# Kernel optimization log

Measured on AMD Instinct MI355X. Metric: run time of the kernel, lower is better.

The kernel has to match this reference:

```python
import math
import jax, jax.numpy as jnp
import numpy as np

DIM = 1024
NUM_HEADS = 16
HEAD_DIM = DIM // NUM_HEADS


def rotate_half(x):
    x1, x2 = jnp.split(x, 2, axis=-1)
    return jnp.concatenate((-x2, x1), axis=-1)


def rope_cos_sin(seq_len, head_dim, dtype):
    # angles: (S, D/2); duplicated to (S, D) so it applies to full head_dim
    pos = jnp.arange(seq_len, dtype=dtype)[:, None]
    inv = jnp.exp(jnp.arange(0, head_dim, 2, dtype=dtype) * (-(math.log(10000.0) / head_dim)))
    angles = pos * inv[None, :]
    angles = jnp.concatenate((angles, angles), axis=-1)  # (S, D)
    return jnp.cos(angles), jnp.sin(angles)


def setup_inputs() -> dict:
    key = jax.random.key(0)
    ks = jax.random.split(key, 5)
    B, S, C = 8, 1024, DIM
    scale = 1.0 / math.sqrt(C)
    return {
        "x": jax.random.normal(ks[0], (B, S, C), dtype=jnp.float32),
        "W_qkv": jax.random.normal(ks[1], (C, 3 * C), dtype=jnp.float32) * scale,
        "b_qkv": jax.random.normal(ks[2], (3 * C,), dtype=jnp.float32) * 0.02,
        "W_proj": jax.random.normal(ks[3], (C, C), dtype=jnp.float32) * scale,
        "b_proj": jax.random.normal(ks[4], (C,), dtype=jnp.float32) * 0.02,
    }


def reference(x, W_qkv, b_qkv, W_proj, b_proj):
    B, S, C = x.shape
    H, D = NUM_HEADS, C // NUM_HEADS
    scale = D ** -0.5

    qkv = x @ W_qkv + b_qkv                       # (B, S, 3C)
    qkv = qkv.reshape(B, S, 3, H, D).transpose(2, 0, 3, 1, 4)  # (3, B, H, S, D)
    q, k, v = qkv[0], qkv[1], qkv[2]

    cos, sin = rope_cos_sin(S, D, x.dtype)        # (S, D) each, broadcast over B,H
    q = q * cos + rotate_half(q) * sin
    k = k * cos + rotate_half(k) * sin

    attn = jnp.einsum("bhqd,bhkd->bhqk", q, k) * scale
    attn = jax.nn.softmax(attn, axis=-1)
    out = jnp.einsum("bhqk,bhkd->bhqd", attn, v)  # (B, H, S, D)
    out = out.transpose(0, 2, 1, 3).reshape(B, S, C)
    return out @ W_proj + b_proj
```

## Files before the change

### kernel.cpp

```cpp
#include <hip/hip_runtime.h>
#include <hip/hip_fp16.h>
#include <math.h>


typedef _Float16 half_t;
typedef _Float16 half8 __attribute__((ext_vector_type(8)));
typedef _Float16 half4v __attribute__((ext_vector_type(4)));
typedef float f32x4 __attribute__((ext_vector_type(4)));

#define MFMA16(a, b, c) __builtin_amdgcn_mfma_f32_16x16x32_f16(a, b, c, 0, 0, 0)

__device__ __forceinline__ void gload_lds16(const half_t* g, half_t* lds) {
  __builtin_amdgcn_global_load_lds(
      (const __attribute__((address_space(1))) void*)g,
      (__attribute__((address_space(3))) void*)lds, 16, 0, 0);
}

__device__ __forceinline__ void prep_transpose(const float* __restrict__ in,
                                               half_t* __restrict__ out,
                                               int rows, int cols, int bx,
                                               int by, half_t (*tile)[33]) {
  int c0 = bx * 32, r0 = by * 32;
  int tx = threadIdx.x & 31, g = threadIdx.x >> 5;
#pragma unroll
  for (int i = 0; i < 4; i++) {
    int r = g * 4 + i;
    tile[r][tx] = (half_t)in[(size_t)(r0 + r) * cols + c0 + tx];
  }
  __syncthreads();
#pragma unroll
  for (int i = 0; i < 4; i++) {
    int cc = g * 4 + i;
    out[(size_t)(c0 + cc) * rows + r0 + tx] = tile[tx][cc];
  }
}

__global__ __launch_bounds__(256) void k_prep(
    const float* __restrict__ x, half_t* __restrict__ x16,
    const float* __restrict__ Wqkv, half_t* __restrict__ WqkvT,
    const float* __restrict__ Wproj, half_t* __restrict__ WprojT,
    float2* __restrict__ rope) {
  __shared__ half_t tile[32][33];
  int bid = blockIdx.x;
  if (bid < 8192) {
    int i = bid * 256 + threadIdx.x;
    float4 v = ((const float4*)x)[i];
    half4v h;
    h.x = (half_t)v.x; h.y = (half_t)v.y; h.z = (half_t)v.z; h.w = (half_t)v.w;
    ((half4v*)x16)[i] = h;
  } else if (bid < 11264) {
    int idx = bid - 8192;
    prep_transpose(Wqkv, WqkvT, 1024, 3072, idx % 96, idx / 96, tile);
  } else if (bid < 12288) {
    int idx = bid - 11264;
    prep_transpose(Wproj, WprojT, 1024, 1024, idx & 31, idx >> 5, tile);
  } else {
    int idx = (bid - 12288) * 256 + threadIdx.x;
    int s = idx >> 5, jj = idx & 31;
    float inv = expf(-0.28782313662425572f * (float)jj);
    float ang = (float)s * inv;
    float sn, cs;
    sincosf(ang, &sn, &cs);
    rope[idx] = make_float2(cs, sn);
  }
}

template <int MODE>
__global__ __launch_bounds__(256) void k_gemm(
    const half_t* __restrict__ A, const half_t* __restrict__ Bt,
    const float* __restrict__ bias, const float2* __restrict__ rope,
    half_t* __restrict__ Qo, half_t* __restrict__ Ko, half_t* __restrict__ Vo,
    float* __restrict__ Fo) {
  __shared__ alignas(16) half_t smem[17408];
  half_t* As = smem;
  half_t* Bs = smem + 8192;
  const int t = threadIdx.x;
  const int lane = t & 63, w = t >> 6;
  const int quad = lane >> 4, cl = lane & 15;
  const int m0 = blockIdx.y * 128, n0 = blockIdx.x * 128;
  const int wm = (w >> 1) * 64, wn = (w & 1) * 64;

  f32x4 acc[4][4] = {};

  for (int kt = 0; kt < 1024; kt += 64) {
    __syncthreads();
#pragma unroll
    for (int cc = 0; cc < 4; cc++) {
      int lg = (w * 4 + cc) * 64 + lane;
      int row = lg >> 3;
      int gs = (lg & 7) ^ (row & 7);
      gload_lds16(A + (size_t)(m0 + row) * 1024 + kt + gs * 8,
                  As + (w * 4 + cc) * 512);
      gload_lds16(Bt + (size_t)(n0 + row) * 1024 + kt + gs * 8,
                  Bs + (w * 4 + cc) * 512);
    }
    __syncthreads();
#pragma unroll
    for (int ks = 0; ks < 2; ks++) {
      half8 af[4], bf[4];
#pragma unroll
      for (int i = 0; i < 4; i++) {
        int mr = wm + i * 16 + cl;
        af[i] = *(const half8*)(As + mr * 64 + (((ks * 4 + quad) ^ (mr & 7)) * 8));
        int nr = wn + i * 16 + cl;
        bf[i] = *(const half8*)(Bs + nr * 64 + (((ks * 4 + quad) ^ (nr & 7)) * 8));
      }
#pragma unroll
      for (int i = 0; i < 4; i++)
#pragma unroll
        for (int j = 0; j < 4; j++) acc[i][j] = MFMA16(af[i], bf[j], acc[i][j]);
    }
  }

  if (MODE == 0) {
    const int which = n0 >> 10;
    if (which == 2) {
      __syncthreads();
      half_t* T = smem;
#pragma unroll
      for (int i = 0; i < 4; i++)
#pragma unroll
        for (int j = 0; j < 4; j++)
#pragma unroll
          for (int r = 0; r < 4; r++) {
            int n = n0 + wn + j * 16 + cl;
            T[(wn + j * 16 + cl) * 136 + (wm + i * 16 + quad * 4 + r)] =
                (half_t)(acc[i][j][r] + bias[n]);
          }
      __syncthreads();
      const int b = m0 >> 10, sbase = m0 & 1023;
#pragma unroll
      for (int u = 0; u < 8; u++) {
        int ci = u * 256 + t;
        int drow = ci >> 4, scol = (ci & 15) * 8;
        half8 val = *(const half8*)(T + drow * 136 + scol);
        int n = n0 + drow;
        int hh = (n >> 6) & 15, d = n & 63;
        *(half8*)(Vo + ((size_t)((b * 16 + hh) * 64 + d)) * 1024 + sbase + scol) = val;
      }
    } else {
      __syncthreads();
      half_t* T = smem;
      const float qsc = (which == 0) ? 0.125f : 1.0f;
#pragma unroll
      for (int i = 0; i < 4; i++)
#pragma unroll
        for (int r = 0; r < 4; r++) {
          int ml = wm + i * 16 + quad * 4 + r;
          int s = (m0 + ml) & 1023;
#pragma unroll
          for (int j = 0; j < 4; j++) {
            int nl = wn + j * 16 + cl;
            int n = n0 + nl;
            int d = n & 63;
            float v = acc[i][j][r] + bias[n];
            float pr = acc[i][j ^ 2][r] + bias[n ^ 32];
            float2 tr = rope[(s << 5) | (d & 31)];
            float rv = (d < 32) ? (v * tr.x - pr * tr.y) : (v * tr.x + pr * tr.y);
            T[ml * 136 + nl] = (half_t)(rv * qsc);
          }
        }
      __syncthreads();
      half_t* dst = (which == 0) ? Qo : Ko;
      const int b = m0 >> 10;
#pragma unroll
      for (int u = 0; u < 8; u++) {
        int ci = u * 256 + t;
        int mrow = ci >> 4, ch = ci & 15;
        half8 val = *(const half8*)(T + mrow * 136 + ch * 8);
        int s = (m0 + mrow) & 1023;
        int n = n0 + ch * 8;
        int hh = (n >> 6) & 15, d = n & 63;
        *(half8*)(dst + ((size_t)((b * 16 + hh) * 1024 + s)) * 64 + d) = val;
      }
    }
  } else {
#pragma unroll
    for (int i = 0; i < 4; i++)
#pragma unroll
      for (int r = 0; r < 4; r++) {
        int gm = m0 + wm + i * 16 + quad * 4 + r;
#pragma unroll
        for (int j = 0; j < 4; j++) {
          int n = n0 + wn + j * 16 + cl;
          Fo[(size_t)gm * 1024 + n] = acc[i][j][r] + bias[n];
        }
      }
  }
}

__global__ __launch_bounds__(256) void k_attn(const half_t* __restrict__ Qg_,
                                              const half_t* __restrict__ Kg_,
                                              const half_t* __restrict__ Vg_,
                                              half_t* __restrict__ Og) {
  __shared__ alignas(16) half_t Qs[8192];
  __shared__ alignas(16) half_t Ks[4096];
  __shared__ alignas(16) half_t Vs[4096];
  __shared__ alignas(16) half_t Ps[128 * 72];
  __shared__ float ilbuf[128];
  const int t = threadIdx.x, lane = t & 63, w = t >> 6;
  const int quad = lane >> 4, cl = lane & 15;
  const int bh = blockIdx.x, q0 = blockIdx.y * 128;
  const half_t* Qg = Qg_ + (size_t)bh * 65536;
  const half_t* Kg = Kg_ + (size_t)bh * 65536;
  const half_t* Vg = Vg_ + (size_t)bh * 65536;

#pragma unroll
  for (int cc = 0; cc < 4; cc++) {
    int lg = (w * 4 + cc) * 64 + lane;
    int row = lg >> 3;
    int gs = (lg & 7) ^ (row & 7);
    gload_lds16(Qg + (size_t)(q0 + row) * 64 + gs * 8, Qs + (w * 4 + cc) * 512);
  }
  __syncthreads();

  half8 qf[2][2];
#pragma unroll
  for (int ks = 0; ks < 2; ks++)
#pragma unroll
    for (int j = 0; j < 2; j++) {
      int qr = w * 32 + j * 16 + cl;
      qf[ks][j] = *(const half8*)(Qs + qr * 64 + (((ks * 4 + quad) ^ (qr & 7)) * 8));
    }

  f32x4 oacc[2][4] = {};
  float lsum[2] = {0.f, 0.f};

  for (int kt = 0; kt < 1024; kt += 64) {
    __syncthreads();
#pragma unroll
    for (int cc = 0; cc < 2; cc++) {
      int lg = (w * 2 + cc) * 64 + lane;
      int row = lg >> 3;
      int gs = (lg & 7) ^ (row & 7);
      gload_lds16(Kg + (size_t)(kt + row) * 64 + gs * 8, Ks + (w * 2 + cc) * 512);
      gload_lds16(Vg + (size_t)row * 1024 + kt + gs * 8, Vs + (w * 2 + cc) * 512);
    }
    __syncthreads();

    f32x4 sacc[4][2] = {};
#pragma unroll
    for (int ks = 0; ks < 2; ks++) {
      half8 kf[4];
#pragma unroll
      for (int i = 0; i < 4; i++) {
        int kr = i * 16 + cl;
        kf[i] = *(const half8*)(Ks + kr * 64 + (((ks * 4 + quad) ^ (kr & 7)) * 8));
      }
#pragma unroll
      for (int i = 0; i < 4; i++)
#pragma unroll
        for (int j = 0; j < 2; j++)
          sacc[i][j] = MFMA16(kf[i], qf[ks][j], sacc[i][j]);
    }

#pragma unroll
    for (int i = 0; i < 4; i++)
#pragma unroll
      for (int j = 0; j < 2; j++) {
        float p0 = __expf(sacc[i][j][0] - 8.f);
        float p1 = __expf(sacc[i][j][1] - 8.f);
        float p2 = __expf(sacc[i][j][2] - 8.f);
        float p3 = __expf(sacc[i][j][3] - 8.f);
        lsum[j] += (p0 + p1) + (p2 + p3);
        half4v pk;
        pk.x = (half_t)p0; pk.y = (half_t)p1; pk.z = (half_t)p2; pk.w = (half_t)p3;
        *(half4v*)(Ps + (w * 32 + j * 16 + cl) * 72 + i * 16 + quad * 4) = pk;
      }

#pragma unroll
    for (int ks = 0; ks < 2; ks++) {
      half8 pf[2], vf[4];
#pragma unroll
      for (int i = 0; i < 2; i++)
        pf[i] = *(const half8*)(Ps + (w * 32 + i * 16 + cl) * 72 + ks * 32 + quad * 8);
#pragma unroll
      for (int j = 0; j < 4; j++) {
        int dr = j * 16 + cl;
        vf[j] = *(const half8*)(Vs + dr * 64 + (((ks * 4 + quad) ^ (dr & 7)) * 8));
      }
#pragma unroll
      for (int i = 0; i < 2; i++)
#pragma unroll
        for (int j = 0; j < 4; j++) oacc[i][j] = MFMA16(pf[i], vf[j], oacc[i][j]);
    }
  }

#pragma unroll
  for (int j = 0; j < 2; j++) {
    float l = lsum[j];
    l += __shfl_xor(l, 16);
    l += __shfl_xor(l, 32);
    if (quad == 0) ilbuf[w * 32 + j * 16 + cl] = 1.f / l;
  }

  const int b = bh >> 4, hh = bh & 15;
#pragma unroll
  for (int i = 0; i < 2; i++)
#pragma unroll
    for (int r = 0; r < 4; r++) {
      float sc = ilbuf[w * 32 + i * 16 + quad * 4 + r];
      int srow = q0 + w * 32 + i * 16 + quad * 4 + r;
#pragma unroll
      for (int j = 0; j < 4; j++) {
        int d = j * 16 + cl;
        Og[((size_t)(b * 1024 + srow)) * 1024 + hh * 64 + d] =
            (half_t)(oacc[i][j][r] * sc);
      }
    }
}

extern "C" void kernel_launch(void* const* d_in, const int* in_sizes, int n_in,
                              void* d_out, int out_size, void* d_ws,
                              size_t ws_size, hipStream_t stream) {
  (void)in_sizes; (void)n_in; (void)out_size; (void)ws_size;
  const float* x = (const float*)d_in[0];
  const float* Wqkv = (const float*)d_in[1];
  const float* bqkv = (const float*)d_in[2];
  const float* Wproj = (const float*)d_in[3];
  const float* bproj = (const float*)d_in[4];
  float* out = (float*)d_out;

  half_t* ws = (half_t*)d_ws;
  half_t* x16 = ws;
  half_t* WqkvT = ws + 8388608;
  half_t* WprojT = ws + 11534336;
  half_t* Q16 = ws + 12582912;
  half_t* K16 = ws + 20971520;
  half_t* V16 = ws + 29360128;
  float2* rope = (float2*)(ws + 37748736);
  half_t* O16 = x16;

  k_prep<<<12416, 256, 0, stream>>>(x, x16, Wqkv, WqkvT, Wproj, WprojT, rope);
  k_gemm<0><<<dim3(24, 64), 256, 0, stream>>>(x16, WqkvT, bqkv, rope, Q16, K16,
                                              V16, nullptr);
  k_attn<<<dim3(128, 8), 256, 0, stream>>>(Q16, K16, V16, O16);
  k_gemm<1><<<dim3(8, 64), 256, 0, stream>>>(O16, WprojT, bproj, nullptr,
                                             nullptr, nullptr, nullptr, out);
}
```

Baseline: 246.9 us.

## Replace QKV GEMM with 256x256-tile double-buffered 512-thread kernel

Adds a dedicated QKV projection kernel that uses 256x256 output tiles with 8 waves per block. It double-buffers K-slices in LDS via direct global-to-LDS loads interleaved with the MFMA phases, and remaps blocks to a swizzled grid order for L2 locality. The goal is more data reuse per loaded byte and overlap of loads with MFMA compute than the old 128x128 single-buffered GEMM. In exchange it uses 128 KB of LDS and many more accumulator registers, and the epilogue is split into two halves through LDS.

```diff
diff --git a/kernel.cpp b/kernel.cpp
--- a/kernel.cpp
+++ b/kernel.cpp
@@ -65,6 +65,159 @@
   }
 }
 
+
+#define STAGE_HALF(TT, PH)                                                   \
+  {                                                                          \
+    const int op_ = (PH) & 1, kh_ = (PH) >> 1;                               \
+    const half_t* src_ = op_ ? Bt : A;                                       \
+    const int r0_ = op_ ? n0 : m0;                                           \
+    half_t* reg_ = smem + (((TT) & 1) * 32768) + op_ * 16384 + kh_ * 8192;   \
+    _Pragma("unroll") for (int c_ = 0; c_ < 2; ++c_) {                       \
+      int gid_ = c_ * 512 + w * 64 + lane;                                   \
+      int row_ = gid_ >> 2, gi_ = gid_ & 3;                                  \
+      int sg_ = gi_ ^ ((row_ >> 1) & 3);                                     \
+      gload_lds16(src_ + (size_t)(r0_ + row_) * 1024 + (TT) * 64 +           \
+                      kh_ * 32 + sg_ * 8,                                    \
+                  reg_ + (c_ * 512 + w * 64) * 8);                           \
+    }                                                                        \
+  }
+
+__global__ __launch_bounds__(512, 2) void k_qkv(
+    const half_t* __restrict__ A, const half_t* __restrict__ Bt,
+    const float* __restrict__ bias, const float2* __restrict__ rope,
+    half_t* __restrict__ Qo, half_t* __restrict__ Ko,
+    half_t* __restrict__ Vo) {
+  __shared__ alignas(16) half_t smem[65536];
+  const int t = threadIdx.x;
+  const int lane = t & 63, w = t >> 6;
+  const int quad = lane >> 4, cl = lane & 15;
+  const int wr = w >> 2, wc = w & 3;
+
+  const int bid = blockIdx.x;
+  const int wg = (bid & 7) * 48 + (bid >> 3);
+  const int m0 = (wg & 31) * 256, n0 = (wg >> 5) * 256;
+
+#pragma unroll
+  for (int ph = 0; ph < 4; ++ph) STAGE_HALF(0, ph);
+  asm volatile("s_waitcnt vmcnt(4)" ::: "memory");
+  __builtin_amdgcn_s_barrier();
+
+  f32x4 acc[8][4] = {};
+  half8 bf[4];
+
+  for (int tt = 0; tt < 16; ++tt) {
+    half_t* Ab = smem + (tt & 1) * 32768;
+    half_t* Bb = Ab + 16384;
+#pragma unroll
+    for (int ph = 0; ph < 4; ++ph) {
+      const int ks = ph >> 1, mh = ph & 1;
+      if (mh == 0) {
+#pragma unroll
+        for (int j = 0; j < 4; ++j) {
+          int nr = wc * 64 + j * 16 + cl;
+          bf[j] = *(const half8*)(Bb + ks * 8192 + nr * 32 +
+                                  ((quad ^ ((nr >> 1) & 3)) * 8));
+        }
+      }
+      half8 af[4];
+#pragma unroll
+      for (int i = 0; i < 4; ++i) {
+        int mr = wr * 128 + mh * 64 + i * 16 + cl;
+        af[i] = *(const half8*)(Ab + ks * 8192 + mr * 32 +
+                                ((quad ^ ((mr >> 1) & 3)) * 8));
+      }
+      if (tt < 15) STAGE_HALF(tt + 1, ph);
+      __builtin_amdgcn_s_barrier();
+      asm volatile("s_waitcnt lgkmcnt(0)" ::: "memory");
+      __builtin_amdgcn_sched_barrier(0);
+      __builtin_amdgcn_s_setprio(1);
+#pragma unroll
+      for (int i = 0; i < 4; ++i)
+#pragma unroll
+        for (int j = 0; j < 4; ++j)
+          acc[mh * 4 + i][j] = MFMA16(af[i], bf[j], acc[mh * 4 + i][j]);
+      __builtin_amdgcn_s_setprio(0);
+      if (ph & 1) {
+        if (tt < 15)
+          asm volatile("s_waitcnt vmcnt(4)" ::: "memory");
+        else
+          asm volatile("s_waitcnt vmcnt(0)" ::: "memory");
+      }
+      __builtin_amdgcn_s_barrier();
+    }
+  }
+
+  const int which = n0 >> 10;
+  const int b = m0 >> 10, sbase = m0 & 1023;
+  if (which == 2) {
+    half_t* T = smem;
+    for (int rm = 0; rm < 2; ++rm) {
+      if (rm) __syncthreads();
+      if (wr == rm) {
+#pragma unroll
+        for (int mi = 0; mi < 8; ++mi)
+#pragma unroll
+          for (int j = 0; j < 4; ++j) {
+            int nl = wc * 64 + j * 16 + cl;
+            float bs = bias[n0 + nl];
+#pragma unroll
+            for (int r = 0; r < 4; ++r)
+              T[nl * 136 + mi * 16 + quad * 4 + r] =
+                  (half_t)(acc[mi][j][r] + bs);
+          }
+      }
+      __syncthreads();
+#pragma unroll
+      for (int u = 0; u < 8; ++u) {
+        int ci = u * 512 + t;
+        int nl = ci >> 4, ch = (ci & 15) * 8;
+        half8 val = *(const half8*)(T + nl * 136 + ch);
+        int n = n0 + nl, hh = (n >> 6) & 15, d = n & 63;
+        *(half8*)(Vo + ((size_t)((b * 16 + hh) * 64 + d)) * 1024 + sbase +
+                  rm * 128 + ch) = val;
+      }
+    }
+  } else {
+    half_t* T = smem;
+    const float qsc = (which == 0) ? 0.125f : 1.0f;
+    half_t* dst = (which == 0) ? Qo : Ko;
+    for (int rm = 0; rm < 2; ++rm) {
+      if (rm) __syncthreads();
+      if (wr == rm) {
+#pragma unroll
+        for (int mi = 0; mi < 8; ++mi)
+#pragma unroll
+          for (int r = 0; r < 4; ++r) {
+            int tl = mi * 16 + quad * 4 + r;
+            int s = sbase + rm * 128 + tl;
+#pragma unroll
+            for (int j = 0; j < 4; ++j) {
+              int nl = wc * 64 + j * 16 + cl;
+              int n = n0 + nl, d = n & 63;
+              float v = acc[mi][j][r] + bias[n];
+              float pr = acc[mi][j ^ 2][r] + bias[n ^ 32];
+              float2 tr = rope[(s << 5) | (d & 31)];
+              float rv =
+                  (d < 32) ? (v * tr.x - pr * tr.y) : (v * tr.x + pr * tr.y);
+              T[tl * 264 + nl] = (half_t)(rv * qsc);
+            }
+          }
+      }
+      __syncthreads();
+#pragma unroll
+      for (int u = 0; u < 8; ++u) {
+        int ci = u * 512 + t;
+        int mrow = ci >> 5, ch = (ci & 31) * 8;
+        half8 val = *(const half8*)(T + mrow * 264 + ch);
+        int s = sbase + rm * 128 + mrow;
+        int n = n0 + ch, hh = (n >> 6) & 15, d = n & 63;
+        *(half8*)(dst + ((size_t)((b * 16 + hh) * 1024 + s)) * 64 + d) = val;
+      }
+    }
+  }
+}
+#undef STAGE_HALF
+
 template <int MODE>
 __global__ __launch_bounds__(256) void k_gemm(
     const half_t* __restrict__ A, const half_t* __restrict__ Bt,
@@ -112,81 +265,17 @@
     }
   }
 
-  if (MODE == 0) {
-    const int which = n0 >> 10;
-    if (which == 2) {
-      __syncthreads();
-      half_t* T = smem;
-#pragma unroll
-      for (int i = 0; i < 4; i++)
-#pragma unroll
-        for (int j = 0; j < 4; j++)
-#pragma unroll
-          for (int r = 0; r < 4; r++) {
-            int n = n0 + wn + j * 16 + cl;
-            T[(wn + j * 16 + cl) * 136 + (wm + i * 16 + quad * 4 + r)] =
-                (half_t)(acc[i][j][r] + bias[n]);
-          }
-      __syncthreads();
-      const int b = m0 >> 10, sbase = m0 & 1023;
-#pragma unroll
-      for (int u = 0; u < 8; u++) {
-        int ci = u * 256 + t;
-        int drow = ci >> 4, scol = (ci & 15) * 8;
-        half8 val = *(const half8*)(T + drow * 136 + scol);
-        int n = n0 + drow;
-        int hh = (n >> 6) & 15, d = n & 63;
-        *(half8*)(Vo + ((size_t)((b * 16 + hh) * 64 + d)) * 1024 + sbase + scol) = val;
-      }
-    } else {
-      __syncthreads();
-      half_t* T = smem;
-      const float qsc = (which == 0) ? 0.125f : 1.0f;
-#pragma unroll
-      for (int i = 0; i < 4; i++)
-#pragma unroll
-        for (int r = 0; r < 4; r++) {
-          int ml = wm + i * 16 + quad * 4 + r;
-          int s = (m0 + ml) & 1023;
-#pragma unroll
-          for (int j = 0; j < 4; j++) {
-            int nl = wn + j * 16 + cl;
-            int n = n0 + nl;
-            int d = n & 63;
-            float v = acc[i][j][r] + bias[n];
-            float pr = acc[i][j ^ 2][r] + bias[n ^ 32];
-            float2 tr = rope[(s << 5) | (d & 31)];
-            float rv = (d < 32) ? (v * tr.x - pr * tr.y) : (v * tr.x + pr * tr.y);
-            T[ml * 136 + nl] = (half_t)(rv * qsc);
-          }
-        }
-      __syncthreads();
-      half_t* dst = (which == 0) ? Qo : Ko;
-      const int b = m0 >> 10;
-#pragma unroll
-      for (int u = 0; u < 8; u++) {
-        int ci = u * 256 + t;
-        int mrow = ci >> 4, ch = ci & 15;
-        half8 val = *(const half8*)(T + mrow * 136 + ch * 8);
-        int s = (m0 + mrow) & 1023;
-        int n = n0 + ch * 8;
-        int hh = (n >> 6) & 15, d = n & 63;
-        *(half8*)(dst + ((size_t)((b * 16 + hh) * 1024 + s)) * 64 + d) = val;
-      }
-    }
-  } else {
-#pragma unroll
-    for (int i = 0; i < 4; i++)
-#pragma unroll
-      for (int r = 0; r < 4; r++) {
-        int gm = m0 + wm + i * 16 + quad * 4 + r;
-#pragma unroll
-        for (int j = 0; j < 4; j++) {
-          int n = n0 + wn + j * 16 + cl;
-          Fo[(size_t)gm * 1024 + n] = acc[i][j][r] + bias[n];
-        }
-      }
-  }
+#pragma unroll
+  for (int i = 0; i < 4; i++)
+#pragma unroll
+    for (int r = 0; r < 4; r++) {
+      int gm = m0 + wm + i * 16 + quad * 4 + r;
+#pragma unroll
+      for (int j = 0; j < 4; j++) {
+        int n = n0 + wn + j * 16 + cl;
+        Fo[(size_t)gm * 1024 + n] = acc[i][j][r] + bias[n];
+      }
+    }
 }
 
 __global__ __launch_bounds__(256) void k_attn(const half_t* __restrict__ Qg_,
@@ -332,8 +421,7 @@
   half_t* O16 = x16;
 
   k_prep<<<12416, 256, 0, stream>>>(x, x16, Wqkv, WqkvT, Wproj, WprojT, rope);
-  k_gemm<0><<<dim3(24, 64), 256, 0, stream>>>(x16, WqkvT, bqkv, rope, Q16, K16,
-                                              V16, nullptr);
+  k_qkv<<<384, 512, 0, stream>>>(x16, WqkvT, bqkv, rope, Q16, K16, V16);
   k_attn<<<dim3(128, 8), 256, 0, stream>>>(Q16, K16, V16, O16);
   k_gemm<1><<<dim3(8, 64), 256, 0, stream>>>(O16, WprojT, bproj, nullptr,
                                              nullptr, nullptr, nullptr, out);
```

Result: slower. 301.1 us (+21.9%).
